# Kernel tuning notes

Hardware: AMD Instinct MI355X
Metric: run time of the kernel (lower is better)

## Reference

```python
import jax, jax.numpy as jnp
import numpy as np

NCH, NBASIS, NXS, NF = 8, 30, 256, 200
NX = NXS * NXS * 2  # flattened real-pair k-space length


def _fft2c(z):
    # centered orthonormal 2D FFT over the last two axes
    z = jnp.fft.ifftshift(z, axes=(-2, -1))
    z = jnp.fft.fft2(z, norm='ortho')
    return jnp.fft.fftshift(z, axes=(-2, -1))


def setup_inputs() -> dict:
    key = jax.random.key(0)
    k1, k2, k3, k4 = jax.random.split(key, 4)
    x = jax.random.normal(k1, (NBASIS, NXS, NXS, 2), dtype=jnp.float32)
    csmT = jax.random.normal(k2, (NCH, NXS, NXS, 2), dtype=jnp.float32)
    VT = jax.random.normal(k3, (NBASIS, NF), dtype=jnp.float32)
    maskT = jax.random.randint(k4, (NF, NX), 0, 2).astype(jnp.bool_)
    return {"x": x, "csmT": csmT, "VT": VT, "maskT": maskT}


def reference(x, csmT, VT, maskT):
    # x: (nbasis, nx, nx, 2) real-pair complex; csmT: (nch, nx, nx, 2)
    xc = jax.lax.complex(x[..., 0], x[..., 1])          # (b, nx, nx)
    cc = jax.lax.complex(csmT[..., 0], csmT[..., 1])    # (c, nx, nx)
    # coil-sensitivity weighting + centered FFT, batched over all coils/basis
    Y = _fft2c(xc[None, :, :, :] * cc[:, None, :, :])   # (c, b, nx, nx) complex
    # interleave real/imag to match torch reshape of (..., nx, nx, 2) -> (..., NX)
    Yr = jnp.stack([Y.real, Y.imag], axis=-1).reshape(NCH, NBASIS, NX)
    # per-frame subspace projection then mask (mask commutes with the b-sum)
    out = maskT[None, :, :].astype(Yr.dtype) * jnp.einsum('cbn,bf->cfn', Yr, VT)
    return out  # (nch, NF, NX)
```

## Files before the change

### kernel.cpp

```cpp
#include <hip/hip_runtime.h>

#define NCH    8
#define NBASIS 30
#define NXS    256
#define NF     200
#define NX     (NXS*NXS*2)
#define NIMG   (NCH*NBASIS)
#define NFT    13

typedef float    f32x4  __attribute__((ext_vector_type(4)));
typedef unsigned u32x4  __attribute__((ext_vector_type(4)));
typedef short    bf16x8 __attribute__((ext_vector_type(8)));

__device__ __forceinline__ int bitrev8(int v) {
    return (int)(__builtin_bitreverse32((unsigned)v) >> 24);
}

__device__ __forceinline__ unsigned short f2bf(float f) {
    unsigned u = __float_as_uint(f);
    return (unsigned short)((u + 0x7FFFu + ((u >> 16) & 1u)) >> 16);
}

__global__ __launch_bounds__(256) void fft_rows_kernel(
        const float* __restrict__ x, const float* __restrict__ csm,
        unsigned short* __restrict__ Amid) {
    __shared__ float ldsRe[4][256];
    __shared__ float ldsIm[4][256];
    __shared__ float twRe[128], twIm[128];

    const int tid   = threadIdx.x;
    const int slice = tid >> 6;
    const int lane  = tid & 63;
    const int blk   = blockIdx.x;
    const int m     = blk >> 6;
    const int row   = ((blk & 63) << 2) + slice;
    const int c     = m / NBASIS;
    const int b     = m - c * NBASIS;

    if (tid < 128) {
        float a = (float)tid * (1.0f / 128.0f);
        twRe[tid] =  cospif(a);
        twIm[tid] = -sinpif(a);
    }

    const float* xr = x   + ((size_t)(b * NXS + row) * NXS) * 2;
    const float* cr = csm + ((size_t)(c * NXS + row) * NXS) * 2;
    #pragma unroll
    for (int j = 0; j < 4; ++j) {
        int col = lane + 64 * j;
        float2 xv = *(const float2*)(xr + col * 2);
        float2 cv = *(const float2*)(cr + col * 2);
        float s = ((row + col) & 1) ? -1.0f : 1.0f;
        ldsRe[slice][col] = s * (xv.x * cv.x - xv.y * cv.y);
        ldsIm[slice][col] = s * (xv.x * cv.y + xv.y * cv.x);
    }
    __syncthreads();

    #pragma unroll
    for (int half = 128; half >= 1; half >>= 1) {
        #pragma unroll
        for (int qq = 0; qq < 2; ++qq) {
            int q  = lane + 64 * qq;
            int g  = q / half;
            int j  = q - g * half;
            int i0 = g * 2 * half + j;
            int i1 = i0 + half;
            float ar = ldsRe[slice][i0], ai = ldsIm[slice][i0];
            float br = ldsRe[slice][i1], bi = ldsIm[slice][i1];
            ldsRe[slice][i0] = ar + br;
            ldsIm[slice][i0] = ai + bi;
            float dr = ar - br, di = ai - bi;
            int k = j * (128 / half);
            float wr = twRe[k], wi = twIm[k];
            ldsRe[slice][i1] = dr * wr - di * wi;
            ldsIm[slice][i1] = dr * wi + di * wr;
        }
        __syncthreads();
    }

    unsigned short* outp = Amid + (size_t)m * NX + (size_t)row * NXS * 2;
    #pragma unroll
    for (int j = 0; j < 4; ++j) {
        int k  = lane + 64 * j;
        int rk = bitrev8(k);
        unsigned pack = (unsigned)f2bf(ldsRe[slice][rk])
                      | ((unsigned)f2bf(ldsIm[slice][rk]) << 16);
        *(unsigned*)(outp + k * 2) = pack;
    }
}

#define CTILE 16
__global__ __launch_bounds__(256) void fft_cols_kernel(
        const unsigned short* __restrict__ Amid, unsigned short* __restrict__ Abf) {
    __shared__ float ldsRe[CTILE][257];
    __shared__ float ldsIm[CTILE][257];
    __shared__ float twRe[128], twIm[128];

    const int tid = threadIdx.x;
    const int blk = blockIdx.x;
    const int m   = blk >> 4;
    const int k0  = (blk & 15) * CTILE;

    if (tid < 128) {
        float a = (float)tid * (1.0f / 128.0f);
        twRe[tid] =  cospif(a);
        twIm[tid] = -sinpif(a);
    }

    const unsigned short* base = Amid + (size_t)m * NX;
    #pragma unroll
    for (int it = 0; it < 16; ++it) {
        int li = it * 256 + tid;
        int r  = li >> 4;
        int cc = li & 15;
        unsigned v = *(const unsigned*)(base + ((size_t)r * NXS + k0 + cc) * 2);
        ldsRe[cc][r] = __uint_as_float(v << 16);
        ldsIm[cc][r] = __uint_as_float(v & 0xFFFF0000u);
    }
    __syncthreads();

    const int slice = tid >> 6;
    const int lane  = tid & 63;

    #pragma unroll
    for (int half = 128; half >= 1; half >>= 1) {
        #pragma unroll
        for (int ci = 0; ci < 4; ++ci) {
            int col = slice * 4 + ci;
            #pragma unroll
            for (int qq = 0; qq < 2; ++qq) {
                int q  = lane + 64 * qq;
                int g  = q / half;
                int j  = q - g * half;
                int i0 = g * 2 * half + j;
                int i1 = i0 + half;
                float ar = ldsRe[col][i0], ai = ldsIm[col][i0];
                float br = ldsRe[col][i1], bi = ldsIm[col][i1];
                ldsRe[col][i0] = ar + br;
                ldsIm[col][i0] = ai + bi;
                float dr = ar - br, di = ai - bi;
                int k = j * (128 / half);
                float wr = twRe[k], wi = twIm[k];
                ldsRe[col][i1] = dr * wr - di * wi;
                ldsIm[col][i1] = dr * wi + di * wr;
            }
        }
        __syncthreads();
    }

    unsigned short* obase = Abf + (size_t)m * NX;
    #pragma unroll
    for (int it = 0; it < 16; ++it) {
        int li = it * 256 + tid;
        int ky = li >> 4;
        int cc = li & 15;
        int kx = k0 + cc;
        int rk = bitrev8(ky);
        float s = (((ky + kx) & 1) ? -1.0f : 1.0f) * (1.0f / 256.0f);
        unsigned pack = ((unsigned)f2bf(s * ldsIm[cc][rk]) << 16)
                      |  (unsigned)f2bf(s * ldsRe[cc][rk]);
        *(unsigned*)(obase + ((size_t)ky * NXS + kx) * 2) = pack;
    }
}

__global__ __launch_bounds__(256) void vt_prep_kernel(
        const float* __restrict__ VT, unsigned short* __restrict__ VTfrag) {
    int i = blockIdx.x * 256 + threadIdx.x;
    if (i >= NFT * 512) return;
    int ft = i >> 9, r = i & 511, lane = r >> 3, j = r & 7;
    int k = (lane >> 4) * 8 + j;
    int f = ft * 16 + (lane & 15);
    unsigned short v = 0;
    if (k < NBASIS && f < NF) v = f2bf(VT[k * NF + f]);
    VTfrag[i] = v;
}

__global__ __launch_bounds__(256) void project_mfma_kernel(
        const unsigned short* __restrict__ Abf,
        const unsigned short* __restrict__ VTfrag,
        const void*           __restrict__ maskT,
        float* __restrict__ out) {
    __shared__ __align__(16) unsigned char smem[4][4864];

    const int tid  = threadIdx.x;
    const int wv   = tid >> 6;
    const int lane = tid & 63;
    const int ksec = lane >> 4;
    const int fr   = lane & 15;
    const int c    = blockIdx.y;
    const int n0w  = blockIdx.x * 256 + wv * 64;

    const unsigned* mwd = (const unsigned*)maskT;
    bool byteMode = false;
    #pragma unroll
    for (int i = 0; i < 32; ++i) byteMode |= (mwd[i] > 1u);

    unsigned short (*ylds)[72] = (unsigned short (*)[72])smem[wv];
    float          (*ldsW)[68] = (float (*)[68])smem[wv];

    {
        const unsigned short* src = Abf + (size_t)c * NBASIS * NX + n0w;
        #pragma unroll
        for (int i = 0; i < 4; ++i) {
            int idx = lane + 64 * i;
            int row = idx >> 3, seg = idx & 7;
            u32x4 v = (u32x4)(0u, 0u, 0u, 0u);
            if (row < NBASIS)
                v = *(const u32x4*)(src + (size_t)row * NX + seg * 8);
            *(u32x4*)&ylds[row][seg * 8] = v;
        }
    }
    __builtin_amdgcn_wave_barrier();
    asm volatile("s_waitcnt lgkmcnt(0)" ::: "memory");
    __builtin_amdgcn_sched_barrier(0);

    bf16x8 yfrag[4];
    #pragma unroll
    for (int fn = 0; fn < 4; ++fn) {
        #pragma unroll
        for (int j = 0; j < 8; ++j)
            yfrag[fn][j] = (short)ylds[ksec * 8 + j][fn * 16 + fr];
    }
    __builtin_amdgcn_wave_barrier();
    asm volatile("s_waitcnt lgkmcnt(0)" ::: "memory");
    __builtin_amdgcn_sched_barrier(0);

    const unsigned short* vtp = VTfrag + lane * 8;
    float* outc = out + (size_t)c * NF * NX;

    #pragma unroll 1
    for (int ft = 0; ft < NFT; ++ft) {
        bf16x8 vt = *(const bf16x8*)(vtp + ft * 512);

        const int  f_l = ft * 16 + fr;
        const bool fok = f_l < NF;
        unsigned md[4];
        if (byteMode) {
            const unsigned char* mb = (const unsigned char*)maskT
                + (size_t)f_l * NX + n0w + ksec * 4;
            #pragma unroll
            for (int fn = 0; fn < 4; ++fn)
                md[fn] = fok ? *(const unsigned*)(mb + fn * 16) : 0u;
        } else {
            const int* mi = (const int*)maskT + (size_t)f_l * NX + n0w + ksec * 4;
            #pragma unroll
            for (int fn = 0; fn < 4; ++fn) {
                unsigned m = 0;
                if (fok) {
                    u32x4 v = *(const u32x4*)(mi + fn * 16);
                    m = (v.x ? 1u : 0u) | (v.y ? 0x100u : 0u)
                      | (v.z ? 0x10000u : 0u) | (v.w ? 0x1000000u : 0u);
                }
                md[fn] = m;
            }
        }

        #pragma unroll
        for (int fn = 0; fn < 4; ++fn) {
            f32x4 d = __builtin_amdgcn_mfma_f32_16x16x32_bf16(
                yfrag[fn], vt, (f32x4)(0.f, 0.f, 0.f, 0.f), 0, 0, 0);
            f32x4 o;
            #pragma unroll
            for (int r = 0; r < 4; ++r)
                o[r] = ((md[fn] >> (8 * r)) & 0xFFu) ? d[r] : 0.0f;
            *(f32x4*)&ldsW[fr][fn * 16 + ksec * 4] = o;
        }
        __builtin_amdgcn_wave_barrier();
        asm volatile("s_waitcnt lgkmcnt(0)" ::: "memory");
        __builtin_amdgcn_sched_barrier(0);

        #pragma unroll
        for (int rl = 0; rl < 4; ++rl) {
            int f_local = rl * 4 + ksec;
            int f = ft * 16 + f_local;
            f32x4 v = *(const f32x4*)&ldsW[f_local][fr * 4];
            if (f < NF)
                __builtin_nontemporal_store(v,
                    (f32x4*)(outc + (size_t)f * NX + n0w + fr * 4));
        }
        __builtin_amdgcn_wave_barrier();
    }
}

extern "C" void kernel_launch(void* const* d_in, const int* in_sizes, int n_in,
                              void* d_out, int out_size, void* d_ws, size_t ws_size,
                              hipStream_t stream) {
    const float* x    = (const float*)d_in[0];
    const float* csm  = (const float*)d_in[1];
    const float* VT   = (const float*)d_in[2];
    const void*  mask = d_in[3];
    float* out = (float*)d_out;

    char* ws = (char*)d_ws;
    unsigned short* Amid   = (unsigned short*)ws;
    unsigned short* Abf    = (unsigned short*)(ws + ((size_t)64 << 20));
    unsigned short* VTfrag = (unsigned short*)(ws + ((size_t)128 << 20));

    vt_prep_kernel<<<(NFT * 512 + 255) / 256, 256, 0, stream>>>(VT, VTfrag);
    fft_rows_kernel<<<NIMG * 64, 256, 0, stream>>>(x, csm, Amid);
    fft_cols_kernel<<<NIMG * 16, 256, 0, stream>>>(Amid, Abf);
    project_mfma_kernel<<<dim3(NX / 256, NCH), 256, 0, stream>>>(Abf, VTfrag, mask, out);
}
```

Measured before the change: 392.7 us.

## Reuse compressed mask bits across four coils per projection block

Each projection block now handles four coils instead of one. The mask for its n-range is loaded once, packed into a 208-bit register bitmap, and reused for all four coils, so the mask no longer has to be reread per coil. VT fragments are also staged in LDS, and the frame loop is fully unrolled. This cuts redundant mask traffic, which is large in the int path, but it reduces the grid by four, raises register and LDS use, and serialises the coils within each block.

```diff
diff --git a/kernel.cpp b/kernel.cpp
--- a/kernel.cpp
+++ b/kernel.cpp
@@ -7,6 +7,7 @@
 #define NX     (NXS*NXS*2)
 #define NIMG   (NCH*NBASIS)
 #define NFT    13
+#define CPB    4
 
 typedef float    f32x4  __attribute__((ext_vector_type(4)));
 typedef unsigned u32x4  __attribute__((ext_vector_type(4)));
@@ -181,104 +182,130 @@
         const void*           __restrict__ maskT,
         float* __restrict__ out) {
     __shared__ __align__(16) unsigned char smem[4][4864];
+    __shared__ __align__(16) unsigned short vtlds[NFT * 512];
 
     const int tid  = threadIdx.x;
     const int wv   = tid >> 6;
     const int lane = tid & 63;
     const int ksec = lane >> 4;
     const int fr   = lane & 15;
-    const int c    = blockIdx.y;
+    const int c0   = blockIdx.y * CPB;
     const int n0w  = blockIdx.x * 256 + wv * 64;
+
+    {
+        const u32x4* src = (const u32x4*)VTfrag;
+        u32x4*       dst = (u32x4*)vtlds;
+        for (int i = tid; i < NFT * 512 / 8; i += 256) dst[i] = src[i];
+    }
 
     const unsigned* mwd = (const unsigned*)maskT;
     bool byteMode = false;
     #pragma unroll
     for (int i = 0; i < 32; ++i) byteMode |= (mwd[i] > 1u);
 
+    unsigned mbits[7] = {0u, 0u, 0u, 0u, 0u, 0u, 0u};
+    if (byteMode) {
+        const unsigned char* mb = (const unsigned char*)maskT + n0w + ksec * 4;
+        #pragma unroll
+        for (int ft = 0; ft < NFT; ++ft) {
+            const int f_l = ft * 16 + fr;
+            #pragma unroll
+            for (int fn = 0; fn < 4; ++fn) {
+                unsigned w = (f_l < NF)
+                    ? *(const unsigned*)(mb + (size_t)f_l * NX + fn * 16) : 0u;
+                unsigned nib = (w | (w >> 7) | (w >> 14) | (w >> 21)) & 0xFu;
+                const int p = ft * 16 + fn * 4;
+                mbits[p >> 5] |= nib << (p & 31);
+            }
+        }
+    } else {
+        const int* mi = (const int*)maskT + n0w + ksec * 4;
+        #pragma unroll
+        for (int ft = 0; ft < NFT; ++ft) {
+            const int f_l = ft * 16 + fr;
+            #pragma unroll
+            for (int fn = 0; fn < 4; ++fn) {
+                unsigned nib = 0u;
+                if (f_l < NF) {
+                    u32x4 v = *(const u32x4*)(mi + (size_t)f_l * NX + fn * 16);
+                    nib = (v.x ? 1u : 0u) | (v.y ? 2u : 0u)
+                        | (v.z ? 4u : 0u) | (v.w ? 8u : 0u);
+                }
+                const int p = ft * 16 + fn * 4;
+                mbits[p >> 5] |= nib << (p & 31);
+            }
+        }
+    }
+
     unsigned short (*ylds)[72] = (unsigned short (*)[72])smem[wv];
     float          (*ldsW)[68] = (float (*)[68])smem[wv];
 
-    {
-        const unsigned short* src = Abf + (size_t)c * NBASIS * NX + n0w;
-        #pragma unroll
-        for (int i = 0; i < 4; ++i) {
-            int idx = lane + 64 * i;
-            int row = idx >> 3, seg = idx & 7;
-            u32x4 v = (u32x4)(0u, 0u, 0u, 0u);
-            if (row < NBASIS)
-                v = *(const u32x4*)(src + (size_t)row * NX + seg * 8);
-            *(u32x4*)&ylds[row][seg * 8] = v;
-        }
-    }
-    __builtin_amdgcn_wave_barrier();
-    asm volatile("s_waitcnt lgkmcnt(0)" ::: "memory");
-    __builtin_amdgcn_sched_barrier(0);
-
-    bf16x8 yfrag[4];
-    #pragma unroll
-    for (int fn = 0; fn < 4; ++fn) {
-        #pragma unroll
-        for (int j = 0; j < 8; ++j)
-            yfrag[fn][j] = (short)ylds[ksec * 8 + j][fn * 16 + fr];
-    }
-    __builtin_amdgcn_wave_barrier();
-    asm volatile("s_waitcnt lgkmcnt(0)" ::: "memory");
-    __builtin_amdgcn_sched_barrier(0);
-
-    const unsigned short* vtp = VTfrag + lane * 8;
-    float* outc = out + (size_t)c * NF * NX;
+    __syncthreads();
 
     #pragma unroll 1
-    for (int ft = 0; ft < NFT; ++ft) {
-        bf16x8 vt = *(const bf16x8*)(vtp + ft * 512);
-
-        const int  f_l = ft * 16 + fr;
-        const bool fok = f_l < NF;
-        unsigned md[4];
-        if (byteMode) {
-            const unsigned char* mb = (const unsigned char*)maskT
-                + (size_t)f_l * NX + n0w + ksec * 4;
-            #pragma unroll
-            for (int fn = 0; fn < 4; ++fn)
-                md[fn] = fok ? *(const unsigned*)(mb + fn * 16) : 0u;
-        } else {
-            const int* mi = (const int*)maskT + (size_t)f_l * NX + n0w + ksec * 4;
-            #pragma unroll
-            for (int fn = 0; fn < 4; ++fn) {
-                unsigned m = 0;
-                if (fok) {
-                    u32x4 v = *(const u32x4*)(mi + fn * 16);
-                    m = (v.x ? 1u : 0u) | (v.y ? 0x100u : 0u)
-                      | (v.z ? 0x10000u : 0u) | (v.w ? 0x1000000u : 0u);
-                }
-                md[fn] = m;
-            }
-        }
-
-        #pragma unroll
-        for (int fn = 0; fn < 4; ++fn) {
-            f32x4 d = __builtin_amdgcn_mfma_f32_16x16x32_bf16(
-                yfrag[fn], vt, (f32x4)(0.f, 0.f, 0.f, 0.f), 0, 0, 0);
-            f32x4 o;
-            #pragma unroll
-            for (int r = 0; r < 4; ++r)
-                o[r] = ((md[fn] >> (8 * r)) & 0xFFu) ? d[r] : 0.0f;
-            *(f32x4*)&ldsW[fr][fn * 16 + ksec * 4] = o;
+    for (int cc = 0; cc < CPB; ++cc) {
+        const int c = c0 + cc;
+
+        {
+            const unsigned short* src = Abf + (size_t)c * NBASIS * NX + n0w;
+            #pragma unroll
+            for (int i = 0; i < 4; ++i) {
+                int idx = lane + 64 * i;
+                int row = idx >> 3, seg = idx & 7;
+                u32x4 v = (u32x4)(0u, 0u, 0u, 0u);
+                if (row < NBASIS)
+                    v = *(const u32x4*)(src + (size_t)row * NX + seg * 8);
+                *(u32x4*)&ylds[row][seg * 8] = v;
+            }
         }
         __builtin_amdgcn_wave_barrier();
         asm volatile("s_waitcnt lgkmcnt(0)" ::: "memory");
         __builtin_amdgcn_sched_barrier(0);
 
-        #pragma unroll
-        for (int rl = 0; rl < 4; ++rl) {
-            int f_local = rl * 4 + ksec;
-            int f = ft * 16 + f_local;
-            f32x4 v = *(const f32x4*)&ldsW[f_local][fr * 4];
-            if (f < NF)
-                __builtin_nontemporal_store(v,
-                    (f32x4*)(outc + (size_t)f * NX + n0w + fr * 4));
+        bf16x8 yfrag[4];
+        #pragma unroll
+        for (int fn = 0; fn < 4; ++fn) {
+            #pragma unroll
+            for (int j = 0; j < 8; ++j)
+                yfrag[fn][j] = (short)ylds[ksec * 8 + j][fn * 16 + fr];
         }
         __builtin_amdgcn_wave_barrier();
+        asm volatile("s_waitcnt lgkmcnt(0)" ::: "memory");
+        __builtin_amdgcn_sched_barrier(0);
+
+        float* outc = out + (size_t)c * NF * NX;
+
+        #pragma unroll
+        for (int ft = 0; ft < NFT; ++ft) {
+            bf16x8 vt = *(const bf16x8*)&vtlds[ft * 512 + lane * 8];
+
+            #pragma unroll
+            for (int fn = 0; fn < 4; ++fn) {
+                const int p = ft * 16 + fn * 4;
+                const unsigned nib = (mbits[p >> 5] >> (p & 31)) & 0xFu;
+                f32x4 d = __builtin_amdgcn_mfma_f32_16x16x32_bf16(
+                    yfrag[fn], vt, (f32x4)(0.f, 0.f, 0.f, 0.f), 0, 0, 0);
+                f32x4 o;
+                #pragma unroll
+                for (int r = 0; r < 4; ++r)
+                    o[r] = (nib & (1u << r)) ? d[r] : 0.0f;
+                *(f32x4*)&ldsW[fr][fn * 16 + ksec * 4] = o;
+            }
+            __builtin_amdgcn_wave_barrier();
+            asm volatile("s_waitcnt lgkmcnt(0)" ::: "memory");
+            __builtin_amdgcn_sched_barrier(0);
+
+            #pragma unroll
+            for (int rl = 0; rl < 4; ++rl) {
+                int f_local = rl * 4 + ksec;
+                int f = ft * 16 + f_local;
+                f32x4 v = *(const f32x4*)&ldsW[f_local][fr * 4];
+                if (f < NF)
+                    __builtin_nontemporal_store(v,
+                        (f32x4*)(outc + (size_t)f * NX + n0w + fr * 4));
+            }
+            __builtin_amdgcn_wave_barrier();
+        }
     }
 }
 
@@ -299,5 +326,6 @@
     vt_prep_kernel<<<(NFT * 512 + 255) / 256, 256, 0, stream>>>(VT, VTfrag);
     fft_rows_kernel<<<NIMG * 64, 256, 0, stream>>>(x, csm, Amid);
     fft_cols_kernel<<<NIMG * 16, 256, 0, stream>>>(Amid, Abf);
-    project_mfma_kernel<<<dim3(NX / 256, NCH), 256, 0, stream>>>(Abf, VTfrag, mask, out);
-}
+    project_mfma_kernel<<<dim3(NX / 256, NCH / CPB), 256, 0, stream>>>(
+        Abf, VTfrag, mask, out);
+}
```

Measured after the change: 327.0 us. 16.7% less time.
